# Optimization experiments

Hardware: AMD Instinct MI355X
Metric: run time of the kernel (lower is better)

The kernel has to match this reference:

```python
import jax, jax.numpy as jnp
import numpy as np

N_SRC, N_MID, N_OUT = 100000, 20000, 5000
E1, E2 = 20000, 20000
IN, H, EF = 64, 64, 32


def setup_inputs() -> dict:
    key = jax.random.key(0)
    ks = jax.random.split(key, 12)
    s = 1.0 / np.sqrt(EF)
    return {
        "in_feat": jax.random.normal(ks[0], (N_SRC, IN), jnp.float32),
        "edge_feats": jax.random.normal(ks[1], (E1, EF), jnp.float32),
        "edge_feats1": jax.random.normal(ks[2], (E2, EF), jnp.float32),
        "W1": jax.random.uniform(ks[3], (EF, IN * H), jnp.float32, -s, s),
        "b1": jax.random.uniform(ks[4], (IN * H,), jnp.float32, -s, s),
        "W2": jax.random.uniform(ks[5], (EF, H * H), jnp.float32, -s, s),
        "b2": jax.random.uniform(ks[6], (H * H,), jnp.float32, -s, s),
        "src1": jax.random.randint(ks[7], (E1,), 0, N_SRC, jnp.int32),
        "dst1": jax.random.randint(ks[8], (E1,), 0, N_MID, jnp.int32),
        "src2": jax.random.randint(ks[9], (E2,), 0, N_MID, jnp.int32),
        "dst2": jax.random.randint(ks[10], (E2,), 0, N_OUT, jnp.int32),
    }


def nnconv_mean(h, efeat, W, b, src, dst, n_dst, d_in, d_out):
    # per-edge weight matrix from edge MLP: [E, d_in, d_out]
    We = (efeat @ W + b).reshape(-1, d_in, d_out)
    # gather src feats and apply per-edge matmul: [E, d_out]
    msg = jnp.einsum("ei,eio->eo", h[src], We)
    # scatter-mean into dst nodes (empty dst -> 0, matching DGL mean)
    sums = jax.ops.segment_sum(msg, dst, num_segments=n_dst)
    cnt = jax.ops.segment_sum(jnp.ones((dst.shape[0],), msg.dtype), dst,
                              num_segments=n_dst)
    return sums / jnp.maximum(cnt, 1.0)[:, None]


def reference(in_feat, edge_feats, edge_feats1, W1, b1, W2, b2,
              src1, dst1, src2, dst2):
    h = nnconv_mean(in_feat, edge_feats, W1, b1, src1, dst1, N_MID, IN, H)
    h = jax.nn.relu(h)
    h = nnconv_mean(h, edge_feats1, W2, b2, src2, dst2, N_OUT, H, H)
    return h
```

## Files before the change

### kernel.cpp

```cpp
#include <hip/hip_runtime.h>
#include <hip/hip_bf16.h>

#define N_SRC 100000
#define N_MID 20000
#define N_OUT 5000
#define E_1   20000
#define E_2   20000
#define NCHUNK 33
#define NSPLIT 5
#define EBLK   128
#define NBLK   157
#define EPAD   (NBLK*EBLK)
#define MAXDEG 32

#define PREP_N      (2*NCHUNK*512)
#define PREP_BLKS   ((PREP_N + 255)/256)
#define COUNT_BLKS  ((E_1 + E_2 + 255)/256)

typedef float f32x4 __attribute__((ext_vector_type(4)));
typedef short s16x8 __attribute__((ext_vector_type(8)));

__device__ __forceinline__ void load_lds16(const void* g, void* l) {
    __builtin_amdgcn_global_load_lds(
        (const __attribute__((address_space(1))) unsigned int*)g,
        (__attribute__((address_space(3))) unsigned int*)l, 16, 0, 0);
}

__device__ __forceinline__ s16x8 pack_bf16x8(float4 x, float4 y, float s) {
    union { s16x8 v; __hip_bfloat162 h[4]; } u;
    u.h[0] = __float22bfloat162_rn(make_float2(s * x.x, s * x.y));
    u.h[1] = __float22bfloat162_rn(make_float2(s * x.z, s * x.w));
    u.h[2] = __float22bfloat162_rn(make_float2(s * y.x, s * y.y));
    u.h[3] = __float22bfloat162_rn(make_float2(s * y.z, s * y.w));
    return u.v;
}

__device__ __forceinline__ unsigned short f2bf_rne(float f) {
    unsigned u = __float_as_uint(f);
    return (unsigned short)((u + 0x7FFFu + ((u >> 16) & 1u)) >> 16);
}

__global__ __launch_bounds__(256) void setup_kernel(
    const float* __restrict__ W1, const float* __restrict__ b1,
    const float* __restrict__ W2, const float* __restrict__ b2,
    uint4* __restrict__ Wt1, uint4* __restrict__ Wt2,
    const int* __restrict__ dst1, const int* __restrict__ dst2,
    int* __restrict__ cur1, int* __restrict__ slots1,
    int* __restrict__ cur2, int* __restrict__ slots2)
{
    if (blockIdx.x < PREP_BLKS) {
        int gid = blockIdx.x * 256 + threadIdx.x;
        if (gid >= PREP_N) return;
        int layer = gid / (NCHUNK * 512);
        int r     = gid % (NCHUNK * 512);
        int c  = r / 512;
        int u  = r % 512;
        int k8 = u / 64;
        int n  = u % 64;
        const float* W = layer ? W2 : W1;
        const float* b = layer ? b2 : b1;
        const float* s = (c < 32) ? (W + (size_t)c * 4096) : b;
        union { uint4 v; unsigned short us[8]; } pk;
        #pragma unroll
        for (int j = 0; j < 8; ++j)
            pk.us[j] = f2bf_rne(s[(k8 * 8 + j) * 64 + n]);
        uint4* Wt = layer ? Wt2 : Wt1;
        Wt[(size_t)c * 512 + n * 8 + (k8 ^ (n & 7))] = pk.v;
    } else {
        int i = (blockIdx.x - PREP_BLKS) * 256 + threadIdx.x;
        if (i < E_1) {
            int d = dst1[i];
            int p = atomicAdd(&cur1[d], 1);
            if (p < MAXDEG) slots1[(size_t)d * MAXDEG + p] = i;
        } else if (i < E_1 + E_2) {
            int e = i - E_1;
            int d = dst2[e];
            int p = atomicAdd(&cur2[d], 1);
            if (p < MAXDEG) slots2[(size_t)d * MAXDEG + p] = e;
        }
    }
}

__global__ __launch_bounds__(256) void nnconv_mfma(
    const float* __restrict__ h,
    const float* __restrict__ efeat,
    const uint4* __restrict__ Wt,
    const int*  __restrict__ src,
    int E,
    float* __restrict__ msg)
{
    __shared__ float efs[7][EBLK];
    __shared__ uint4 wbuf[2][512];

    const int t  = threadIdx.x;
    const int w  = t >> 6;
    const int l  = t & 63;
    const int m15 = l & 15;
    const int q   = l >> 4;
    const int ebase = blockIdx.x * EBLK;
    const int split = blockIdx.y;
    const int c_lo = (split * 33) / NSPLIT;
    const int c_hi = ((split + 1) * 33) / NSPLIT;
    const int nc   = c_hi - c_lo;

    for (int idx = t; idx < nc * EBLK; idx += 256) {
        int f = idx >> 7, e = idx & (EBLK - 1);
        int eg = ebase + e, c = c_lo + f;
        float v = 0.0f;
        if (eg < E) v = (c < 32) ? efeat[eg * 32 + c] : 1.0f;
        efs[f][e] = v;
    }

    {
        const uint4* g = Wt + (size_t)c_lo * 512;
        load_lds16(g + t,       &wbuf[0][t]);
        load_lds16(g + 256 + t, &wbuf[0][256 + t]);
    }

    const int e0 = ebase + w * 32 + m15;
    const int e1 = e0 + 16;
    const int r0 = (e0 < E) ? src[e0] : 0;
    const int r1 = (e1 < E) ? src[e1] : 0;
    const float* hp0 = h + (size_t)r0 * 64 + q * 8;
    const float* hp1 = h + (size_t)r1 * 64 + q * 8;
    const float4 t0a0 = *(const float4*)(hp0);
    const float4 t0a1 = *(const float4*)(hp0 + 4);
    const float4 t0b0 = *(const float4*)(hp0 + 32);
    const float4 t0b1 = *(const float4*)(hp0 + 36);
    const float4 t1a0 = *(const float4*)(hp1);
    const float4 t1a1 = *(const float4*)(hp1 + 4);
    const float4 t1b0 = *(const float4*)(hp1 + 32);
    const float4 t1b1 = *(const float4*)(hp1 + 36);

    f32x4 acc0[4] = {};
    f32x4 acc1[4] = {};
    const int nx = m15 & 7;

    int cur = 0;
    for (int c = c_lo; c < c_hi; ++c) {
        __syncthreads();
        if (c + 1 < c_hi) {
            const uint4* g = Wt + (size_t)(c + 1) * 512;
            load_lds16(g + t,       &wbuf[cur ^ 1][t]);
            load_lds16(g + 256 + t, &wbuf[cur ^ 1][256 + t]);
        }
        const float ef0 = efs[c - c_lo][w * 32 + m15];
        const float ef1 = efs[c - c_lo][w * 32 + 16 + m15];
        const s16x8 a00 = pack_bf16x8(t0a0, t0a1, ef0);
        const s16x8 a01 = pack_bf16x8(t0b0, t0b1, ef0);
        const s16x8 a10 = pack_bf16x8(t1a0, t1a1, ef1);
        const s16x8 a11 = pack_bf16x8(t1b0, t1b1, ef1);
        const uint4* wb = wbuf[cur];
        #pragma unroll
        for (int n16 = 0; n16 < 4; ++n16) {
            const int n = n16 * 16 + m15;
            const s16x8 b0 = *(const s16x8*)&wb[n * 8 + ((q)     ^ nx)];
            const s16x8 b1 = *(const s16x8*)&wb[n * 8 + ((4 + q) ^ nx)];
            acc0[n16] = __builtin_amdgcn_mfma_f32_16x16x32_bf16(a00, b0, acc0[n16], 0, 0, 0);
            acc0[n16] = __builtin_amdgcn_mfma_f32_16x16x32_bf16(a01, b1, acc0[n16], 0, 0, 0);
            acc1[n16] = __builtin_amdgcn_mfma_f32_16x16x32_bf16(a10, b0, acc1[n16], 0, 0, 0);
            acc1[n16] = __builtin_amdgcn_mfma_f32_16x16x32_bf16(a11, b1, acc1[n16], 0, 0, 0);
        }
        cur ^= 1;
    }

    float* mp = msg + (size_t)split * EPAD * 64;
    #pragma unroll
    for (int r = 0; r < 4; ++r) {
        float* rp0 = mp + (size_t)(ebase + w * 32 + q * 4 + r) * 64 + m15;
        float* rp1 = rp0 + 16 * 64;
        #pragma unroll
        for (int n16 = 0; n16 < 4; ++n16) {
            rp0[n16 * 16] = acc0[n16][r];
            rp1[n16 * 16] = acc1[n16][r];
        }
    }
}

__global__ __launch_bounds__(256) void gather_mean(
    const float* __restrict__ msg,
    const int* __restrict__ slots, const int* __restrict__ cur,
    int n_dst, int do_relu, float* __restrict__ outp)
{
    int d = blockIdx.x * 4 + (threadIdx.x >> 6);
    int o = threadIdx.x & 63;
    if (d >= n_dst) return;
    int deg = cur[d];
    int dg = min(deg, MAXDEG);
    float s = 0.0f;
    for (int j = 0; j < dg; ++j) {
        int e = slots[(size_t)d * MAXDEG + j];
        const float* mrow = msg + (size_t)e * 64 + o;
        #pragma unroll
        for (int sp = 0; sp < NSPLIT; ++sp)
            s += mrow[(size_t)sp * EPAD * 64];
    }
    s *= 1.0f / fmaxf((float)deg, 1.0f);
    if (do_relu) s = fmaxf(s, 0.0f);
    outp[(size_t)d * 64 + o] = s;
}

extern "C" void kernel_launch(void* const* d_in, const int* in_sizes, int n_in,
                              void* d_out, int out_size, void* d_ws, size_t ws_size,
                              hipStream_t stream)
{
    const float* in_feat = (const float*)d_in[0];
    const float* ef1     = (const float*)d_in[1];
    const float* ef2     = (const float*)d_in[2];
    const float* W1      = (const float*)d_in[3];
    const float* b1      = (const float*)d_in[4];
    const float* W2      = (const float*)d_in[5];
    const float* b2      = (const float*)d_in[6];
    const int*   src1    = (const int*)d_in[7];
    const int*   dst1    = (const int*)d_in[8];
    const int*   src2    = (const int*)d_in[9];
    const int*   dst2    = (const int*)d_in[10];

    float* h_mid  = (float*)d_ws;
    int*   cur1   = (int*)(h_mid + (size_t)N_MID * 64);
    int*   cur2   = cur1 + N_MID;
    int*   slots1 = cur2 + N_OUT;
    int*   slots2 = slots1 + (size_t)N_MID * MAXDEG;
    uint4* Wt1    = (uint4*)(slots2 + (size_t)N_OUT * MAXDEG);
    uint4* Wt2    = Wt1 + (size_t)NCHUNK * 512;
    float* msg    = (float*)(Wt2 + (size_t)NCHUNK * 512);
    float* out    = (float*)d_out;

    hipMemsetAsync(cur1, 0, (size_t)(N_MID + N_OUT) * sizeof(int), stream);

    setup_kernel<<<PREP_BLKS + COUNT_BLKS, 256, 0, stream>>>(
        W1, b1, W2, b2, Wt1, Wt2, dst1, dst2, cur1, slots1, cur2, slots2);

    dim3 grid(NBLK, NSPLIT);
    nnconv_mfma<<<grid, 256, 0, stream>>>(in_feat, ef1, Wt1, src1, E_1, msg);
    gather_mean<<<(N_MID + 3) / 4, 256, 0, stream>>>(msg, slots1, cur1, N_MID, 1, h_mid);

    nnconv_mfma<<<grid, 256, 0, stream>>>(h_mid, ef2, Wt2, src2, E_2, msg);
    gather_mean<<<(N_OUT + 3) / 4, 256, 0, stream>>>(msg, slots2, cur2, N_OUT, 0, out);
}
```

Measured before the change: 159.0 us.

## Fuse all stages into one persistent cooperative kernel with grid syncs

Replaces the memset plus five separate launches (setup, two GEMMs, two gathers) with a single cooperative mega-kernel of 512 persistent blocks. Stages are separated by grid.sync and thread fences, and each block loops over GEMM and gather jobs. The aim is to remove per-launch overhead and inter-kernel gaps, at the cost of grid-wide barrier latency, a fixed grid size and possible load imbalance (785 GEMM jobs over 512 blocks). The edge bucketing now overlaps with the first GEMM stage, which does not depend on the slot lists.

```diff
diff --git a/kernel.cpp b/kernel.cpp
--- a/kernel.cpp
+++ b/kernel.cpp
@@ -1,5 +1,8 @@
 #include <hip/hip_runtime.h>
 #include <hip/hip_bf16.h>
+#include <hip/hip_cooperative_groups.h>
+
+namespace cg = cooperative_groups;
 
 #define N_SRC 100000
 #define N_MID 20000
@@ -12,10 +15,11 @@
 #define NBLK   157
 #define EPAD   (NBLK*EBLK)
 #define MAXDEG 32
-
-#define PREP_N      (2*NCHUNK*512)
-#define PREP_BLKS   ((PREP_N + 255)/256)
-#define COUNT_BLKS  ((E_1 + E_2 + 255)/256)
+#define NJOBS  (NBLK*NSPLIT)
+#define GRID   512
+#define NT     (GRID*256)
+
+#define PREP_N (2*NCHUNK*512)
 
 typedef float f32x4 __attribute__((ext_vector_type(4)));
 typedef short s16x8 __attribute__((ext_vector_type(8)));
@@ -40,54 +44,10 @@
     return (unsigned short)((u + 0x7FFFu + ((u >> 16) & 1u)) >> 16);
 }
 
-__global__ __launch_bounds__(256) void setup_kernel(
-    const float* __restrict__ W1, const float* __restrict__ b1,
-    const float* __restrict__ W2, const float* __restrict__ b2,
-    uint4* __restrict__ Wt1, uint4* __restrict__ Wt2,
-    const int* __restrict__ dst1, const int* __restrict__ dst2,
-    int* __restrict__ cur1, int* __restrict__ slots1,
-    int* __restrict__ cur2, int* __restrict__ slots2)
-{
-    if (blockIdx.x < PREP_BLKS) {
-        int gid = blockIdx.x * 256 + threadIdx.x;
-        if (gid >= PREP_N) return;
-        int layer = gid / (NCHUNK * 512);
-        int r     = gid % (NCHUNK * 512);
-        int c  = r / 512;
-        int u  = r % 512;
-        int k8 = u / 64;
-        int n  = u % 64;
-        const float* W = layer ? W2 : W1;
-        const float* b = layer ? b2 : b1;
-        const float* s = (c < 32) ? (W + (size_t)c * 4096) : b;
-        union { uint4 v; unsigned short us[8]; } pk;
-        #pragma unroll
-        for (int j = 0; j < 8; ++j)
-            pk.us[j] = f2bf_rne(s[(k8 * 8 + j) * 64 + n]);
-        uint4* Wt = layer ? Wt2 : Wt1;
-        Wt[(size_t)c * 512 + n * 8 + (k8 ^ (n & 7))] = pk.v;
-    } else {
-        int i = (blockIdx.x - PREP_BLKS) * 256 + threadIdx.x;
-        if (i < E_1) {
-            int d = dst1[i];
-            int p = atomicAdd(&cur1[d], 1);
-            if (p < MAXDEG) slots1[(size_t)d * MAXDEG + p] = i;
-        } else if (i < E_1 + E_2) {
-            int e = i - E_1;
-            int d = dst2[e];
-            int p = atomicAdd(&cur2[d], 1);
-            if (p < MAXDEG) slots2[(size_t)d * MAXDEG + p] = e;
-        }
-    }
-}
-
-__global__ __launch_bounds__(256) void nnconv_mfma(
-    const float* __restrict__ h,
-    const float* __restrict__ efeat,
-    const uint4* __restrict__ Wt,
-    const int*  __restrict__ src,
-    int E,
-    float* __restrict__ msg)
+__device__ void gemm_job(int job,
+                         const float* __restrict__ h, const float* __restrict__ efeat,
+                         const uint4* __restrict__ Wt, const int* __restrict__ src,
+                         int E, float* __restrict__ msg)
 {
     __shared__ float efs[7][EBLK];
     __shared__ uint4 wbuf[2][512];
@@ -97,11 +57,13 @@
     const int l  = t & 63;
     const int m15 = l & 15;
     const int q   = l >> 4;
-    const int ebase = blockIdx.x * EBLK;
-    const int split = blockIdx.y;
+    const int split = job / NBLK;
+    const int ebase = (job - split * NBLK) * EBLK;
     const int c_lo = (split * 33) / NSPLIT;
     const int c_hi = ((split + 1) * 33) / NSPLIT;
     const int nc   = c_hi - c_lo;
+
+    __syncthreads();
 
     for (int idx = t; idx < nc * EBLK; idx += 256) {
         int f = idx >> 7, e = idx & (EBLK - 1);
@@ -177,14 +139,13 @@
     }
 }
 
-__global__ __launch_bounds__(256) void gather_mean(
-    const float* __restrict__ msg,
-    const int* __restrict__ slots, const int* __restrict__ cur,
-    int n_dst, int do_relu, float* __restrict__ outp)
-{
-    int d = blockIdx.x * 4 + (threadIdx.x >> 6);
-    int o = threadIdx.x & 63;
-    if (d >= n_dst) return;
+__device__ __forceinline__ void gather_job(int d,
+                                           const float* __restrict__ msg,
+                                           const int* __restrict__ slots,
+                                           const int* __restrict__ cur,
+                                           int do_relu, float* __restrict__ outp)
+{
+    const int o = threadIdx.x & 63;
     int deg = cur[d];
     int dg = min(deg, MAXDEG);
     float s = 0.0f;
@@ -198,6 +159,76 @@
     s *= 1.0f / fmaxf((float)deg, 1.0f);
     if (do_relu) s = fmaxf(s, 0.0f);
     outp[(size_t)d * 64 + o] = s;
+}
+
+__global__ __launch_bounds__(256, 2) void mega_kernel(
+    const float* __restrict__ in_feat,
+    const float* __restrict__ ef1, const float* __restrict__ ef2,
+    const float* __restrict__ W1, const float* __restrict__ b1,
+    const float* __restrict__ W2, const float* __restrict__ b2,
+    const int* __restrict__ src1, const int* __restrict__ dst1,
+    const int* __restrict__ src2, const int* __restrict__ dst2,
+    float* __restrict__ h_mid,
+    int* __restrict__ cur1, int* __restrict__ slots1,
+    int* __restrict__ cur2, int* __restrict__ slots2,
+    uint4* __restrict__ Wt1, uint4* __restrict__ Wt2,
+    float* __restrict__ msg, float* __restrict__ out)
+{
+    cg::grid_group grid = cg::this_grid();
+    const int gid = blockIdx.x * 256 + threadIdx.x;
+    const int w   = threadIdx.x >> 6;
+
+    for (int i = gid; i < N_MID + N_OUT; i += NT)
+        cur1[i] = 0;
+    for (int item = gid; item < PREP_N; item += NT) {
+        int layer = item / (NCHUNK * 512);
+        int r     = item % (NCHUNK * 512);
+        int c  = r / 512;
+        int u  = r % 512;
+        int k8 = u / 64;
+        int n  = u % 64;
+        const float* W = layer ? W2 : W1;
+        const float* b = layer ? b2 : b1;
+        const float* s = (c < 32) ? (W + (size_t)c * 4096) : b;
+        union { uint4 v; unsigned short us[8]; } pk;
+        #pragma unroll
+        for (int j = 0; j < 8; ++j)
+            pk.us[j] = f2bf_rne(s[(k8 * 8 + j) * 64 + n]);
+        uint4* Wt = layer ? Wt2 : Wt1;
+        Wt[(size_t)c * 512 + n * 8 + (k8 ^ (n & 7))] = pk.v;
+    }
+    __threadfence();
+    grid.sync();
+
+    for (int i = gid; i < E_1 + E_2; i += NT) {
+        if (i < E_1) {
+            int d = dst1[i];
+            int p = atomicAdd(&cur1[d], 1);
+            if (p < MAXDEG) slots1[(size_t)d * MAXDEG + p] = i;
+        } else {
+            int e = i - E_1;
+            int d = dst2[e];
+            int p = atomicAdd(&cur2[d], 1);
+            if (p < MAXDEG) slots2[(size_t)d * MAXDEG + p] = e;
+        }
+    }
+    for (int job = blockIdx.x; job < NJOBS; job += GRID)
+        gemm_job(job, in_feat, ef1, Wt1, src1, E_1, msg);
+    __threadfence();
+    grid.sync();
+
+    for (int jb = blockIdx.x; jb < N_MID / 4; jb += GRID)
+        gather_job(jb * 4 + w, msg, slots1, cur1, 1, h_mid);
+    __threadfence();
+    grid.sync();
+
+    for (int job = blockIdx.x; job < NJOBS; job += GRID)
+        gemm_job(job, h_mid, ef2, Wt2, src2, E_2, msg);
+    __threadfence();
+    grid.sync();
+
+    for (int jb = blockIdx.x; jb < N_OUT / 4; jb += GRID)
+        gather_job(jb * 4 + w, msg, slots2, cur2, 0, out);
 }
 
 extern "C" void kernel_launch(void* const* d_in, const int* in_sizes, int n_in,
@@ -226,15 +257,13 @@
     float* msg    = (float*)(Wt2 + (size_t)NCHUNK * 512);
     float* out    = (float*)d_out;
 
-    hipMemsetAsync(cur1, 0, (size_t)(N_MID + N_OUT) * sizeof(int), stream);
-
-    setup_kernel<<<PREP_BLKS + COUNT_BLKS, 256, 0, stream>>>(
-        W1, b1, W2, b2, Wt1, Wt2, dst1, dst2, cur1, slots1, cur2, slots2);
-
-    dim3 grid(NBLK, NSPLIT);
-    nnconv_mfma<<<grid, 256, 0, stream>>>(in_feat, ef1, Wt1, src1, E_1, msg);
-    gather_mean<<<(N_MID + 3) / 4, 256, 0, stream>>>(msg, slots1, cur1, N_MID, 1, h_mid);
-
-    nnconv_mfma<<<grid, 256, 0, stream>>>(h_mid, ef2, Wt2, src2, E_2, msg);
-    gather_mean<<<(N_OUT + 3) / 4, 256, 0, stream>>>(msg, slots2, cur2, N_OUT, 0, out);
-}
+    void* args[] = {
+        (void*)&in_feat, (void*)&ef1, (void*)&ef2,
+        (void*)&W1, (void*)&b1, (void*)&W2, (void*)&b2,
+        (void*)&src1, (void*)&dst1, (void*)&src2, (void*)&dst2,
+        (void*)&h_mid, (void*)&cur1, (void*)&slots1, (void*)&cur2, (void*)&slots2,
+        (void*)&Wt1, (void*)&Wt2, (void*)&msg, (void*)&out
+    };
+    hipLaunchCooperativeKernel((void*)mega_kernel, dim3(GRID), dim3(256),
+                               args, 0, stream);
+}
```

Measured after the change: 631.6 us. +297.3%, slower.

## Load per-chunk weights directly into registers instead of LDS double buffer

Applied to the files above, without the earlier changes.

Each wave now loads its slice of the bf16 weight chunk straight from global memory into registers, prefetching the next chunk while computing the current one. This removes the LDS staging buffer, the XOR swizzle and the per-iteration __syncthreads. Each wave now issues its own global (likely L2-cached) weight loads, and register use grows. The number of chunk splits drops from 5 to 4, so each block does more chunks and the grid is smaller.

```diff
diff --git a/kernel.cpp b/kernel.cpp
--- a/kernel.cpp
+++ b/kernel.cpp
@@ -7,7 +7,7 @@
 #define E_1   20000
 #define E_2   20000
 #define NCHUNK 33
-#define NSPLIT 5
+#define NSPLIT 4
 #define EBLK   128
 #define NBLK   157
 #define EPAD   (NBLK*EBLK)
@@ -19,12 +19,6 @@
 
 typedef float f32x4 __attribute__((ext_vector_type(4)));
 typedef short s16x8 __attribute__((ext_vector_type(8)));
-
-__device__ __forceinline__ void load_lds16(const void* g, void* l) {
-    __builtin_amdgcn_global_load_lds(
-        (const __attribute__((address_space(1))) unsigned int*)g,
-        (__attribute__((address_space(3))) unsigned int*)l, 16, 0, 0);
-}
 
 __device__ __forceinline__ s16x8 pack_bf16x8(float4 x, float4 y, float s) {
     union { s16x8 v; __hip_bfloat162 h[4]; } u;
@@ -38,6 +32,10 @@
 __device__ __forceinline__ unsigned short f2bf_rne(float f) {
     unsigned u = __float_as_uint(f);
     return (unsigned short)((u + 0x7FFFu + ((u >> 16) & 1u)) >> 16);
+}
+
+__device__ __forceinline__ s16x8 as_s16x8(uint4 v) {
+    union { uint4 u; s16x8 s; } c; c.u = v; return c.s;
 }
 
 __global__ __launch_bounds__(256) void setup_kernel(
@@ -65,7 +63,7 @@
         for (int j = 0; j < 8; ++j)
             pk.us[j] = f2bf_rne(s[(k8 * 8 + j) * 64 + n]);
         uint4* Wt = layer ? Wt2 : Wt1;
-        Wt[(size_t)c * 512 + n * 8 + (k8 ^ (n & 7))] = pk.v;
+        Wt[(size_t)c * 512 + n * 8 + k8] = pk.v;
     } else {
         int i = (blockIdx.x - PREP_BLKS) * 256 + threadIdx.x;
         if (i < E_1) {
@@ -89,8 +87,7 @@
     int E,
     float* __restrict__ msg)
 {
-    __shared__ float efs[7][EBLK];
-    __shared__ uint4 wbuf[2][512];
+    __shared__ float efs[9][EBLK];
 
     const int t  = threadIdx.x;
     const int w  = t >> 6;
@@ -109,12 +106,6 @@
         float v = 0.0f;
         if (eg < E) v = (c < 32) ? efeat[eg * 32 + c] : 1.0f;
         efs[f][e] = v;
-    }
-
-    {
-        const uint4* g = Wt + (size_t)c_lo * 512;
-        load_lds16(g + t,       &wbuf[0][t]);
-        load_lds16(g + 256 + t, &wbuf[0][256 + t]);
     }
 
     const int e0 = ebase + w * 32 + m15;
@@ -132,36 +123,51 @@
     const float4 t1b0 = *(const float4*)(hp1 + 32);
     const float4 t1b1 = *(const float4*)(hp1 + 36);
 
+    __syncthreads();
+
+    uint4 bcur[8], bnxt[8];
+    {
+        const uint4* wp = Wt + (size_t)c_lo * 512;
+        #pragma unroll
+        for (int n16 = 0; n16 < 4; ++n16) {
+            bcur[n16 * 2 + 0] = wp[(n16 * 16 + m15) * 8 + q];
+            bcur[n16 * 2 + 1] = wp[(n16 * 16 + m15) * 8 + 4 + q];
+        }
+    }
+    float efc0 = efs[0][w * 32 + m15];
+    float efc1 = efs[0][w * 32 + 16 + m15];
+
     f32x4 acc0[4] = {};
     f32x4 acc1[4] = {};
-    const int nx = m15 & 7;
-
-    int cur = 0;
+
     for (int c = c_lo; c < c_hi; ++c) {
-        __syncthreads();
+        float efn0 = 1.0f, efn1 = 1.0f;
         if (c + 1 < c_hi) {
-            const uint4* g = Wt + (size_t)(c + 1) * 512;
-            load_lds16(g + t,       &wbuf[cur ^ 1][t]);
-            load_lds16(g + 256 + t, &wbuf[cur ^ 1][256 + t]);
-        }
-        const float ef0 = efs[c - c_lo][w * 32 + m15];
-        const float ef1 = efs[c - c_lo][w * 32 + 16 + m15];
-        const s16x8 a00 = pack_bf16x8(t0a0, t0a1, ef0);
-        const s16x8 a01 = pack_bf16x8(t0b0, t0b1, ef0);
-        const s16x8 a10 = pack_bf16x8(t1a0, t1a1, ef1);
-        const s16x8 a11 = pack_bf16x8(t1b0, t1b1, ef1);
-        const uint4* wb = wbuf[cur];
+            const uint4* np = Wt + (size_t)(c + 1) * 512;
+            #pragma unroll
+            for (int n16 = 0; n16 < 4; ++n16) {
+                bnxt[n16 * 2 + 0] = np[(n16 * 16 + m15) * 8 + q];
+                bnxt[n16 * 2 + 1] = np[(n16 * 16 + m15) * 8 + 4 + q];
+            }
+            efn0 = efs[c + 1 - c_lo][w * 32 + m15];
+            efn1 = efs[c + 1 - c_lo][w * 32 + 16 + m15];
+        }
+        const s16x8 a00 = pack_bf16x8(t0a0, t0a1, efc0);
+        const s16x8 a01 = pack_bf16x8(t0b0, t0b1, efc0);
+        const s16x8 a10 = pack_bf16x8(t1a0, t1a1, efc1);
+        const s16x8 a11 = pack_bf16x8(t1b0, t1b1, efc1);
         #pragma unroll
         for (int n16 = 0; n16 < 4; ++n16) {
-            const int n = n16 * 16 + m15;
-            const s16x8 b0 = *(const s16x8*)&wb[n * 8 + ((q)     ^ nx)];
-            const s16x8 b1 = *(const s16x8*)&wb[n * 8 + ((4 + q) ^ nx)];
+            const s16x8 b0 = as_s16x8(bcur[n16 * 2 + 0]);
+            const s16x8 b1 = as_s16x8(bcur[n16 * 2 + 1]);
             acc0[n16] = __builtin_amdgcn_mfma_f32_16x16x32_bf16(a00, b0, acc0[n16], 0, 0, 0);
             acc0[n16] = __builtin_amdgcn_mfma_f32_16x16x32_bf16(a01, b1, acc0[n16], 0, 0, 0);
             acc1[n16] = __builtin_amdgcn_mfma_f32_16x16x32_bf16(a10, b0, acc1[n16], 0, 0, 0);
             acc1[n16] = __builtin_amdgcn_mfma_f32_16x16x32_bf16(a11, b1, acc1[n16], 0, 0, 0);
         }
-        cur ^= 1;
+        #pragma unroll
+        for (int j = 0; j < 8; ++j) bcur[j] = bnxt[j];
+        efc0 = efn0; efc1 = efn1;
     }
 
     float* mp = msg + (size_t)split * EPAD * 64;
```

Measured after the change: 178.0 us. 12.0% more time.

## Preload all weight chunks into LDS up front and read edge features into registers

Applied to the files above, without the earlier changes.

The double-buffered per-chunk weight streaming, with a barrier each iteration, is replaced by one bulk async load of all of a split's weight chunks (up to 7×8KB) into LDS, followed by a single barrier. Edge-feature scalars are now read straight from global memory into per-thread registers instead of being staged through LDS. The chunk loop is fully unrolled and launch bounds request 2 blocks per CU. This removes the per-chunk synchronisation and lets all loads overlap, but raises LDS use per block to 56KB and adds strided global reads of edge features.

```diff
diff --git a/kernel.cpp b/kernel.cpp
--- a/kernel.cpp
+++ b/kernel.cpp
@@ -81,7 +81,7 @@
     }
 }
 
-__global__ __launch_bounds__(256) void nnconv_mfma(
+__global__ __launch_bounds__(256, 2) void nnconv_mfma(
     const float* __restrict__ h,
     const float* __restrict__ efeat,
     const uint4* __restrict__ Wt,
@@ -89,8 +89,7 @@
     int E,
     float* __restrict__ msg)
 {
-    __shared__ float efs[7][EBLK];
-    __shared__ uint4 wbuf[2][512];
+    __shared__ uint4 wlds[7 * 512];
 
     const int t  = threadIdx.x;
     const int w  = t >> 6;
@@ -103,18 +102,10 @@
     const int c_hi = ((split + 1) * 33) / NSPLIT;
     const int nc   = c_hi - c_lo;
 
-    for (int idx = t; idx < nc * EBLK; idx += 256) {
-        int f = idx >> 7, e = idx & (EBLK - 1);
-        int eg = ebase + e, c = c_lo + f;
-        float v = 0.0f;
-        if (eg < E) v = (c < 32) ? efeat[eg * 32 + c] : 1.0f;
-        efs[f][e] = v;
-    }
-
     {
         const uint4* g = Wt + (size_t)c_lo * 512;
-        load_lds16(g + t,       &wbuf[0][t]);
-        load_lds16(g + 256 + t, &wbuf[0][256 + t]);
+        for (int u = t; u < nc * 512; u += 256)
+            load_lds16(g + u, &wlds[u]);
     }
 
     const int e0 = ebase + w * 32 + m15;
@@ -132,36 +123,42 @@
     const float4 t1b0 = *(const float4*)(hp1 + 32);
     const float4 t1b1 = *(const float4*)(hp1 + 36);
 
+    float efr0[7], efr1[7];
+    #pragma unroll
+    for (int j = 0; j < 7; ++j) {
+        int c = c_lo + j;
+        float v0 = 0.0f, v1 = 0.0f;
+        if (j < nc) {
+            if (e0 < E) v0 = (c < 32) ? efeat[e0 * 32 + c] : 1.0f;
+            if (e1 < E) v1 = (c < 32) ? efeat[e1 * 32 + c] : 1.0f;
+        }
+        efr0[j] = v0; efr1[j] = v1;
+    }
+
+    __syncthreads();
+
     f32x4 acc0[4] = {};
     f32x4 acc1[4] = {};
     const int nx = m15 & 7;
 
-    int cur = 0;
-    for (int c = c_lo; c < c_hi; ++c) {
-        __syncthreads();
-        if (c + 1 < c_hi) {
-            const uint4* g = Wt + (size_t)(c + 1) * 512;
-            load_lds16(g + t,       &wbuf[cur ^ 1][t]);
-            load_lds16(g + 256 + t, &wbuf[cur ^ 1][256 + t]);
-        }
-        const float ef0 = efs[c - c_lo][w * 32 + m15];
-        const float ef1 = efs[c - c_lo][w * 32 + 16 + m15];
-        const s16x8 a00 = pack_bf16x8(t0a0, t0a1, ef0);
-        const s16x8 a01 = pack_bf16x8(t0b0, t0b1, ef0);
-        const s16x8 a10 = pack_bf16x8(t1a0, t1a1, ef1);
-        const s16x8 a11 = pack_bf16x8(t1b0, t1b1, ef1);
-        const uint4* wb = wbuf[cur];
+    #pragma unroll
+    for (int cc = 0; cc < 7; ++cc) {
+        if (cc >= nc) break;
+        const uint4* wl = wlds + cc * 512;
+        const s16x8 a00 = pack_bf16x8(t0a0, t0a1, efr0[cc]);
+        const s16x8 a01 = pack_bf16x8(t0b0, t0b1, efr0[cc]);
+        const s16x8 a10 = pack_bf16x8(t1a0, t1a1, efr1[cc]);
+        const s16x8 a11 = pack_bf16x8(t1b0, t1b1, efr1[cc]);
         #pragma unroll
         for (int n16 = 0; n16 < 4; ++n16) {
             const int n = n16 * 16 + m15;
-            const s16x8 b0 = *(const s16x8*)&wb[n * 8 + ((q)     ^ nx)];
-            const s16x8 b1 = *(const s16x8*)&wb[n * 8 + ((4 + q) ^ nx)];
+            const s16x8 b0 = *(const s16x8*)&wl[n * 8 + ((q)     ^ nx)];
+            const s16x8 b1 = *(const s16x8*)&wl[n * 8 + ((4 + q) ^ nx)];
             acc0[n16] = __builtin_amdgcn_mfma_f32_16x16x32_bf16(a00, b0, acc0[n16], 0, 0, 0);
             acc0[n16] = __builtin_amdgcn_mfma_f32_16x16x32_bf16(a01, b1, acc0[n16], 0, 0, 0);
             acc1[n16] = __builtin_amdgcn_mfma_f32_16x16x32_bf16(a10, b0, acc1[n16], 0, 0, 0);
             acc1[n16] = __builtin_amdgcn_mfma_f32_16x16x32_bf16(a11, b1, acc1[n16], 0, 0, 0);
         }
-        cur ^= 1;
     }
 
     float* mp = msg + (size_t)split * EPAD * 64;
```

Measured after the change: 161.3 us. About the same (+1.5%).
